# Optimization experiments

Measured on AMD Instinct MI355X. Metric: run time of the kernel, lower is better.

The kernel has to match this reference:

```python
import jax, jax.numpy as jnp
import numpy as np

HIDDEN = 1024

def _cat_linear(x, W, b, cat_ids):
    # x: (B,T,Din), W: (C,Din,Dout), b: (C,Dout)
    return jnp.einsum('bti,bio->bto', x, W[cat_ids]) + b[cat_ids][:, None, :]

def _sinusoidal(timesteps, dim):
    # timesteps: (B,T) int -> (B,T,dim)
    t = timesteps.astype(jnp.float32)
    half = dim // 2
    exponent = -jnp.arange(half, dtype=jnp.float32) * (jnp.log(10000.0) / half)
    freqs = t[..., None] * jnp.exp(exponent)
    return jnp.concatenate([jnp.sin(freqs), jnp.cos(freqs)], axis=-1)

def setup_inputs() -> dict:
    key = jax.random.key(0)
    ks = jax.random.split(key, 8)
    B, T, A, H, C = 64, 64, 64, HIDDEN, 16
    actions = jax.random.normal(ks[0], (B, T, A), dtype=jnp.float32)
    timesteps = jax.random.randint(ks[1], (B,), 0, 1000)
    cat_ids = jax.random.randint(ks[2], (B,), 0, C)
    W1 = 0.02 * jax.random.normal(ks[3], (C, A, H), dtype=jnp.float32)
    b1 = jnp.zeros((C, H), dtype=jnp.float32)
    W2 = 0.02 * jax.random.normal(ks[4], (C, 2 * H, H), dtype=jnp.float32)
    b2 = jnp.zeros((C, H), dtype=jnp.float32)
    W3 = 0.02 * jax.random.normal(ks[5], (C, H, H), dtype=jnp.float32)
    b3 = jnp.zeros((C, H), dtype=jnp.float32)
    return {"actions": actions, "timesteps": timesteps, "cat_ids": cat_ids,
            "W1": W1, "b1": b1, "W2": W2, "b2": b2, "W3": W3, "b3": b3}

def reference(actions, timesteps, cat_ids, W1, b1, W2, b2, W3, b3):
    B, T, _ = actions.shape
    ts = jnp.broadcast_to(timesteps[:, None], (B, T))  # (B,T)
    a_emb = _cat_linear(actions, W1, b1, cat_ids)        # (B,T,H)
    tau = _sinusoidal(ts, HIDDEN).astype(a_emb.dtype)    # (B,T,H)
    x = jnp.concatenate([a_emb, tau], axis=-1)           # (B,T,2H)
    h = _cat_linear(x, W2, b2, cat_ids)
    h = h * jax.nn.sigmoid(h)                            # swish
    return _cat_linear(h, W3, b3, cat_ids)               # (B,T,H)
```

## Files before the change

### kernel.cpp

```cpp
#include <hip/hip_runtime.h>
#include <math.h>


typedef short bf16x8 __attribute__((ext_vector_type(8)));
typedef float floatx4 __attribute__((ext_vector_type(4)));

__device__ inline short f2bf(float f) {
  union { float f; unsigned u; } v; v.f = f;
  unsigned u = v.u;
  return (short)(((u + 0x7fffu + ((u >> 16) & 1u)) >> 16) & 0xffffu);
}

__device__ __forceinline__ unsigned cvtpk(float a, float b) {
  unsigned r;
  asm("v_cvt_pk_bf16_f32 %0, %1, %2" : "=v"(r) : "v"(a), "v"(b));
  return r;
}

#if __has_builtin(__builtin_amdgcn_global_load_lds)
#define ASYNC_LDS 1
__device__ __forceinline__ void async16(const float* g, float* lds) {
  __builtin_amdgcn_global_load_lds(
      (const __attribute__((address_space(1))) unsigned int*)g,
      (__attribute__((address_space(3))) unsigned int*)lds, 16, 0, 0);
}
#else
#define ASYNC_LDS 0
__device__ __forceinline__ void async16(const float* g, float* lds) {
  *(floatx4*)lds = *(const floatx4*)g;
}
#endif

__device__ __forceinline__ void gload16(floatx4& d, const void* p) {
  asm volatile("global_load_dwordx4 %0, %1, off" : "=v"(d) : "v"(p) : "memory");
}
template<int N> __device__ __forceinline__ void vm_wait() {
  asm volatile("s_waitcnt vmcnt(%0)" :: "n"(N) : "memory");
}
__device__ __forceinline__ void lgkm0() {
  asm volatile("s_waitcnt lgkmcnt(0)" ::: "memory");
}

#define KBODY(VMX, LOADA, DOSTAGE, AIN, AOUT)                                  \
  {                                                                            \
    lgkm0();                                                                   \
    if (LOADA) {                                                               \
      _Pragma("unroll")                                                        \
      for (int mt = 0; mt < 8; ++mt) {                                         \
        const char* p = arow[mt] + aoff;                                       \
        if constexpr (A_F32) {                                                 \
          gload16(AOUT[2 * mt], p); gload16(AOUT[2 * mt + 1], p + 16);         \
        } else {                                                               \
          gload16(AOUT[mt], p);                                                \
        }                                                                      \
      }                                                                        \
      aoff += 32 * AB;                                                         \
    }                                                                          \
    if (DOSTAGE) {                                                             \
      _Pragma("unroll")                                                        \
      for (int i = 0; i < 4; ++i)                                              \
        async16((const float*)(wbp + goff[i]), bs + i * 256);                  \
      wbp += 32 * 1024 * 4;                                                    \
    }                                                                          \
    vm_wait<VMX>();                                                            \
    __builtin_amdgcn_sched_barrier(0);                                         \
    bf16x8 af[8];                                                              \
    _Pragma("unroll")                                                          \
    for (int mt = 0; mt < 8; ++mt) {                                           \
      if constexpr (A_F32) {                                                   \
        union { bf16x8 v; unsigned u[4]; } t;                                  \
        floatx4 x0 = AIN[2 * mt], x1 = AIN[2 * mt + 1];                        \
        t.u[0] = cvtpk(x0[0], x0[1]); t.u[1] = cvtpk(x0[2], x0[3]);            \
        t.u[2] = cvtpk(x1[0], x1[1]); t.u[3] = cvtpk(x1[2], x1[3]);            \
        af[mt] = t.v;                                                          \
      } else {                                                                 \
        union { floatx4 f; bf16x8 v; } t; t.f = AIN[mt]; af[mt] = t.v;         \
      }                                                                        \
    }                                                                          \
    _Pragma("unroll")                                                          \
    for (int nt = 0; nt < 2; ++nt) {                                           \
      const float* fp = bc + quad * 256 + ((nt * 16 + l16) ^ (quad << 3));     \
      float f[8];                                                              \
      _Pragma("unroll")                                                        \
      for (int j = 0; j < 8; ++j) f[j] = fp[j * 32];                           \
      union { bf16x8 v; unsigned u[4]; } bb;                                   \
      _Pragma("unroll")                                                        \
      for (int j = 0; j < 4; ++j) bb.u[j] = cvtpk(f[2 * j], f[2 * j + 1]);     \
      _Pragma("unroll")                                                        \
      for (int mt = 0; mt < 8; ++mt)                                           \
        acc[mt][nt] = __builtin_amdgcn_mfma_f32_16x16x32_bf16(                 \
            af[mt], bb.v, acc[mt][nt], 0, 0, 0);                               \
    }                                                                          \
    { float* t_ = bc; bc = bn; bn = bs; bs = t_; }                             \
  }

template<int K, bool A_F32, bool SWISH, bool OUT_BF16, bool TAU>
__global__ __launch_bounds__(256, 2) void gemm_kernel(
    const void* __restrict__ Aall, int lda,
    const float* __restrict__ Wall,
    const float* __restrict__ bias,
    const int* __restrict__ cat_ids,
    void* __restrict__ Out, int ldo,
    const int* __restrict__ ts)
{
  constexpr int NCOL = 1024;
  constexpr int KT = K / 32;
  constexpr int AB = A_F32 ? 4 : 2;
  constexpr int AOPS = A_F32 ? 16 : 8;
#if ASYNC_LDS
  constexpr int VM_MAIN = 8 + AOPS;
  constexpr int VM_T1   = 4 + AOPS;
#else
  constexpr int VM_MAIN = AOPS;
  constexpr int VM_T1   = AOPS;
#endif
  static_assert(KT >= 2 && ((KT - 2) % 2 == 0), "K must be a multiple of 64");
  (void)ts;

  __shared__ float slabs[4][3][1024];
  __shared__ int s_b[80], s_c[80], s_np;

  const int tid = threadIdx.x;
  if (tid < 80) { s_b[tid] = -1; s_c[tid] = 0; }
  __syncthreads();
  if (tid < 64) {
    const int myc = cat_ids[tid];
    int rank = 0, pst = 0, tot = 0;
    #pragma unroll
    for (int cc = 0; cc < 16; ++cc) {
      unsigned long long m = __ballot(myc == cc);
      const int cnt = __popcll(m);
      const int pc  = 2 * ((cnt + 1) >> 1);
      if (cc < myc)  pst += pc;
      if (cc == myc) rank = __popcll(m & ((1ull << tid) - 1ull));
      tot += pc;
    }
    const int slot = pst + rank;
    s_b[slot] = tid;
    s_c[slot] = myc;
    if (tid == 0) s_np = tot >> 1;
  }
  __syncthreads();

  const int e = blockIdx.y;
  if (e >= s_np) return;
  const int b0v = s_b[2 * e];
  int b1 = s_b[2 * e + 1];
  const int c = s_c[2 * e];
  const bool st1 = (b1 >= 0);
  if (!st1) b1 = b0v;

  const int wave = tid >> 6, lane = tid & 63;
  const int quad = lane >> 4, l16 = lane & 15;
  const int ns = blockIdx.x * 128;
  const int wcol = ns + wave * 32;

  const char* arow[8];
  #pragma unroll
  for (int mt = 0; mt < 8; ++mt) {
    const int pr = mt * 16 + l16;
    const int batch = (pr < 64) ? b0v : b1;
    const int row = batch * 64 + (pr & 63);
    arow[mt] = (const char*)Aall + (size_t)row * lda * AB;
  }

  int goff[4];
  #pragma unroll
  for (int i = 0; i < 4; ++i) {
    const int s  = i * 64 + lane;
    const int k  = s >> 3;
    const int c0 = ((s & 7) << 2) ^ ((s >> 6) << 3);
    goff[i] = (k * NCOL + c0) * 4;
  }

  float* const sl0 = &slabs[wave][0][0];
  float* const sl1 = &slabs[wave][1][0];
  float* const sl2 = &slabs[wave][2][0];
  float *bc = sl0, *bn = sl1, *bs = sl2;

  const char* wbp = (const char*)(Wall + (size_t)c * K * NCOL + wcol);

  floatx4 aA[A_F32 ? 16 : 8], aB[A_F32 ? 16 : 8];
  const int aq = quad * 8 * AB;

  #pragma unroll
  for (int mt = 0; mt < 8; ++mt) {
    const char* p = arow[mt] + aq;
    if constexpr (A_F32) { gload16(aA[2 * mt], p); gload16(aA[2 * mt + 1], p + 16); }
    else                 { gload16(aA[mt], p); }
  }
  #pragma unroll
  for (int i = 0; i < 4; ++i) async16((const float*)(wbp + goff[i]), sl0 + i * 256);
  wbp += 32 * NCOL * 4;
  #pragma unroll
  for (int i = 0; i < 4; ++i) async16((const float*)(wbp + goff[i]), sl1 + i * 256);
  wbp += 32 * NCOL * 4;

  int aoff = aq + 32 * AB;

  floatx4 acc[8][2];
  #pragma unroll
  for (int mt = 0; mt < 8; ++mt)
    #pragma unroll
    for (int nt = 0; nt < 2; ++nt)
      acc[mt][nt] = (floatx4){0.f, 0.f, 0.f, 0.f};

  for (int kt = 0; kt + 2 < KT; kt += 2) {
    KBODY(VM_MAIN, true, true, aA, aB);
    KBODY(VM_MAIN, true, true, aB, aA);
  }
  KBODY(VM_T1, true, false, aA, aB);
  KBODY(0, false, false, aB, aA);

  #pragma unroll
  for (int nt = 0; nt < 2; ++nt) {
    const int col = wcol + nt * 16 + l16;
    const float bv = bias[(size_t)c * NCOL + col];
    #pragma unroll
    for (int mt = 0; mt < 8; ++mt) {
      const int prb = mt * 16 + quad * 4;
      const int batch = (prb < 64) ? b0v : b1;
      const bool do_store = (prb < 64) || st1;
      #pragma unroll
      for (int r = 0; r < 4; ++r) {
        const int row = batch * 64 + ((prb + r) & 63);
        float v = acc[mt][nt][r] + bv;
        if constexpr (SWISH) v = v / (1.f + __expf(-v));
        if (do_store) {
          if constexpr (OUT_BF16)
            ((short*)Out)[(size_t)row * ldo + col] = f2bf(v);
          else
            ((float*)Out)[(size_t)row * ldo + col] = v;
        }
      }
    }
  }

  if constexpr (TAU) {
    const float t0  = (float)ts[b0v];
    const float t1v = (float)ts[b1];
    const int ic = ns + (tid & 127);
    const int hi = ic & 511;
    const float ef = __expf(-(float)hi * 0.017988946039015980f);
    float v0, v1;
    if (ic < 512) { v0 = sinf(t0 * ef); v1 = sinf(t1v * ef); }
    else          { v0 = cosf(t0 * ef); v1 = cosf(t1v * ef); }
    const short q0 = f2bf(v0), q1 = f2bf(v1);
    short* xp = (short*)Out;
    const int r0 = tid >> 7;
    #pragma unroll 4
    for (int rr = 0; rr < 32; ++rr) {
      const int rl = r0 + 2 * rr;
      xp[(size_t)(b0v * 64 + rl) * ldo + 1024 + ic] = q0;
      if (st1) xp[(size_t)(b1 * 64 + rl) * ldo + 1024 + ic] = q1;
    }
  }
}

extern "C" void kernel_launch(void* const* d_in, const int* in_sizes, int n_in,
                              void* d_out, int out_size, void* d_ws, size_t ws_size,
                              hipStream_t stream) {
  const float* actions   = (const float*)d_in[0];
  const int*   timesteps = (const int*)  d_in[1];
  const int*   cat_ids   = (const int*)  d_in[2];
  const float* W1 = (const float*)d_in[3];
  const float* B1 = (const float*)d_in[4];
  const float* W2 = (const float*)d_in[5];
  const float* B2 = (const float*)d_in[6];
  const float* W3 = (const float*)d_in[7];
  const float* B3 = (const float*)d_in[8];

  short* x = (short*)d_ws;
  short* h = x + (size_t)64 * 64 * 2048;

  dim3 grid(8, 40), blk(256);

  gemm_kernel<64, true, false, true, true><<<grid, blk, 0, stream>>>(
      (const void*)actions, 64, W1, B1, cat_ids, (void*)x, 2048, timesteps);
  gemm_kernel<2048, false, true, true, false><<<grid, blk, 0, stream>>>(
      (const void*)x, 2048, W2, B2, cat_ids, (void*)h, 1024, nullptr);
  gemm_kernel<1024, false, false, false, false><<<grid, blk, 0, stream>>>(
      (const void*)h, 1024, W3, B3, cat_ids, d_out, 1024, nullptr);
}
```

Before: 432.3 us.

## Load weights directly into registers and halve block size to two waves

Removes the LDS staging of weight tiles: each lane now loads its weight fragments straight from global memory with scalar-base plus vector-offset dword loads, double-buffered in registers. Blocks shrink to 128 threads covering 64 columns, and the grid doubles in x to keep the same coverage. The aim is to cut LDS traffic, its waits and its footprint so more blocks fit per CU. In exchange, the weight loads are strided dword loads rather than wide loads, and register pressure rises.

```diff
diff --git a/kernel.cpp b/kernel.cpp
--- a/kernel.cpp
+++ b/kernel.cpp
@@ -17,85 +17,77 @@
   return r;
 }
 
-#if __has_builtin(__builtin_amdgcn_global_load_lds)
-#define ASYNC_LDS 1
-__device__ __forceinline__ void async16(const float* g, float* lds) {
-  __builtin_amdgcn_global_load_lds(
-      (const __attribute__((address_space(1))) unsigned int*)g,
-      (__attribute__((address_space(3))) unsigned int*)lds, 16, 0, 0);
-}
-#else
-#define ASYNC_LDS 0
-__device__ __forceinline__ void async16(const float* g, float* lds) {
-  *(floatx4*)lds = *(const floatx4*)g;
-}
-#endif
-
-__device__ __forceinline__ void gload16(floatx4& d, const void* p) {
-  asm volatile("global_load_dwordx4 %0, %1, off" : "=v"(d) : "v"(p) : "memory");
-}
-template<int N> __device__ __forceinline__ void vm_wait() {
+template<int IMM>
+__device__ __forceinline__ void gdw(float& d, unsigned voff, unsigned long long base) {
+  asm volatile("global_load_dword %0, %1, %2 offset:%3"
+               : "=v"(d) : "v"(voff), "s"(base), "n"(IMM) : "memory");
+}
+template<int IMM>
+__device__ __forceinline__ void gdx4(floatx4& d, unsigned voff, unsigned long long base) {
+  asm volatile("global_load_dwordx4 %0, %1, %2 offset:%3"
+               : "=v"(d) : "v"(voff), "s"(base), "n"(IMM) : "memory");
+}
+template<int N>
+__device__ __forceinline__ void vm_wait() {
   asm volatile("s_waitcnt vmcnt(%0)" :: "n"(N) : "memory");
 }
-__device__ __forceinline__ void lgkm0() {
-  asm volatile("s_waitcnt lgkmcnt(0)" ::: "memory");
-}
-
-#define KBODY(VMX, LOADA, DOSTAGE, AIN, AOUT)                                  \
-  {                                                                            \
-    lgkm0();                                                                   \
-    if (LOADA) {                                                               \
-      _Pragma("unroll")                                                        \
-      for (int mt = 0; mt < 8; ++mt) {                                         \
-        const char* p = arow[mt] + aoff;                                       \
-        if constexpr (A_F32) {                                                 \
-          gload16(AOUT[2 * mt], p); gload16(AOUT[2 * mt + 1], p + 16);         \
-        } else {                                                               \
-          gload16(AOUT[mt], p);                                                \
-        }                                                                      \
-      }                                                                        \
-      aoff += 32 * AB;                                                         \
-    }                                                                          \
-    if (DOSTAGE) {                                                             \
-      _Pragma("unroll")                                                        \
-      for (int i = 0; i < 4; ++i)                                              \
-        async16((const float*)(wbp + goff[i]), bs + i * 256);                  \
-      wbp += 32 * 1024 * 4;                                                    \
-    }                                                                          \
-    vm_wait<VMX>();                                                            \
-    __builtin_amdgcn_sched_barrier(0);                                         \
-    bf16x8 af[8];                                                              \
-    _Pragma("unroll")                                                          \
-    for (int mt = 0; mt < 8; ++mt) {                                           \
-      if constexpr (A_F32) {                                                   \
-        union { bf16x8 v; unsigned u[4]; } t;                                  \
-        floatx4 x0 = AIN[2 * mt], x1 = AIN[2 * mt + 1];                        \
-        t.u[0] = cvtpk(x0[0], x0[1]); t.u[1] = cvtpk(x0[2], x0[3]);            \
-        t.u[2] = cvtpk(x1[0], x1[1]); t.u[3] = cvtpk(x1[2], x1[3]);            \
-        af[mt] = t.v;                                                          \
-      } else {                                                                 \
-        union { floatx4 f; bf16x8 v; } t; t.f = AIN[mt]; af[mt] = t.v;         \
-      }                                                                        \
-    }                                                                          \
-    _Pragma("unroll")                                                          \
-    for (int nt = 0; nt < 2; ++nt) {                                           \
-      const float* fp = bc + quad * 256 + ((nt * 16 + l16) ^ (quad << 3));     \
-      float f[8];                                                              \
-      _Pragma("unroll")                                                        \
-      for (int j = 0; j < 8; ++j) f[j] = fp[j * 32];                           \
-      union { bf16x8 v; unsigned u[4]; } bb;                                   \
-      _Pragma("unroll")                                                        \
-      for (int j = 0; j < 4; ++j) bb.u[j] = cvtpk(f[2 * j], f[2 * j + 1]);     \
-      _Pragma("unroll")                                                        \
-      for (int mt = 0; mt < 8; ++mt)                                           \
-        acc[mt][nt] = __builtin_amdgcn_mfma_f32_16x16x32_bf16(                 \
-            af[mt], bb.v, acc[mt][nt], 0, 0, 0);                               \
-    }                                                                          \
-    { float* t_ = bc; bc = bn; bn = bs; bs = t_; }                             \
-  }
+
+#define ISSUE_W(WBUF) do {                                                   \
+    _Pragma("unroll")                                                        \
+    for (int j = 0; j < 8; ++j) {                                            \
+      gdw<0 >(WBUF[j],     vW[j], Wq);                                       \
+      gdw<64>(WBUF[8 + j], vW[j], Wq);                                       \
+    }                                                                        \
+    Wq += 32ull * 1024 * 4;                                                  \
+  } while (0)
+
+#define ISSUE_A(ABUF) do {                                                   \
+    _Pragma("unroll")                                                        \
+    for (int mt = 0; mt < 8; ++mt) {                                         \
+      if constexpr (A_F32) {                                                 \
+        gdx4<0 >(ABUF[2 * mt],     vA[mt], Aq);                              \
+        gdx4<16>(ABUF[2 * mt + 1], vA[mt], Aq);                              \
+      } else {                                                               \
+        gdx4<0>(ABUF[mt], vA[mt], Aq);                                       \
+      }                                                                      \
+    }                                                                        \
+    Aq += 32ull * AB;                                                        \
+  } while (0)
+
+#define KSTEP(VM, AIN, AOUT, WIN, DO_A, DO_W) do {                           \
+    vm_wait<VM>();                                                           \
+    __builtin_amdgcn_sched_barrier(0);                                       \
+    union { bf16x8 v; unsigned u[4]; } wb0, wb1;                             \
+    _Pragma("unroll")                                                        \
+    for (int jj = 0; jj < 4; ++jj) {                                         \
+      wb0.u[jj] = cvtpk(WIN[2 * jj],     WIN[2 * jj + 1]);                   \
+      wb1.u[jj] = cvtpk(WIN[8 + 2 * jj], WIN[8 + 2 * jj + 1]);               \
+    }                                                                        \
+    bf16x8 af[8];                                                            \
+    _Pragma("unroll")                                                        \
+    for (int mt = 0; mt < 8; ++mt) {                                         \
+      if constexpr (A_F32) {                                                 \
+        union { bf16x8 v; unsigned u[4]; } t;                                \
+        floatx4 x0 = AIN[2 * mt], x1 = AIN[2 * mt + 1];                      \
+        t.u[0] = cvtpk(x0[0], x0[1]); t.u[1] = cvtpk(x0[2], x0[3]);          \
+        t.u[2] = cvtpk(x1[0], x1[1]); t.u[3] = cvtpk(x1[2], x1[3]);          \
+        af[mt] = t.v;                                                        \
+      } else {                                                               \
+        union { floatx4 f; bf16x8 v; } t; t.f = AIN[mt]; af[mt] = t.v;       \
+      }                                                                      \
+    }                                                                        \
+    __builtin_amdgcn_sched_barrier(0);                                       \
+    if (DO_A) ISSUE_A(AOUT);                                                 \
+    if (DO_W) ISSUE_W(WIN);                                                  \
+    _Pragma("unroll")                                                        \
+    for (int mt = 0; mt < 8; ++mt) {                                         \
+      acc[mt][0] = __builtin_amdgcn_mfma_f32_16x16x32_bf16(af[mt], wb0.v, acc[mt][0], 0, 0, 0); \
+      acc[mt][1] = __builtin_amdgcn_mfma_f32_16x16x32_bf16(af[mt], wb1.v, acc[mt][1], 0, 0, 0); \
+    }                                                                        \
+  } while (0)
 
 template<int K, bool A_F32, bool SWISH, bool OUT_BF16, bool TAU>
-__global__ __launch_bounds__(256, 2) void gemm_kernel(
+__global__ __launch_bounds__(128, 2) void gemm_kernel(
     const void* __restrict__ Aall, int lda,
     const float* __restrict__ Wall,
     const float* __restrict__ bias,
@@ -106,18 +98,9 @@
   constexpr int NCOL = 1024;
   constexpr int KT = K / 32;
   constexpr int AB = A_F32 ? 4 : 2;
-  constexpr int AOPS = A_F32 ? 16 : 8;
-#if ASYNC_LDS
-  constexpr int VM_MAIN = 8 + AOPS;
-  constexpr int VM_T1   = 4 + AOPS;
-#else
-  constexpr int VM_MAIN = AOPS;
-  constexpr int VM_T1   = AOPS;
-#endif
-  static_assert(KT >= 2 && ((KT - 2) % 2 == 0), "K must be a multiple of 64");
+  static_assert(KT >= 2 && ((KT - 2) % 2 == 0), "K must be multiple of 64");
   (void)ts;
 
-  __shared__ float slabs[4][3][1024];
   __shared__ int s_b[80], s_c[80], s_np;
 
   const int tid = threadIdx.x;
@@ -144,73 +127,68 @@
 
   const int e = blockIdx.y;
   if (e >= s_np) return;
-  const int b0v = s_b[2 * e];
-  int b1 = s_b[2 * e + 1];
-  const int c = s_c[2 * e];
+  const int b0v = __builtin_amdgcn_readfirstlane(s_b[2 * e]);
+  int b1        = __builtin_amdgcn_readfirstlane(s_b[2 * e + 1]);
+  const int c   = __builtin_amdgcn_readfirstlane(s_c[2 * e]);
   const bool st1 = (b1 >= 0);
   if (!st1) b1 = b0v;
 
   const int wave = tid >> 6, lane = tid & 63;
   const int quad = lane >> 4, l16 = lane & 15;
-  const int ns = blockIdx.x * 128;
+  const int ns = blockIdx.x * 64;
   const int wcol = ns + wave * 32;
 
-  const char* arow[8];
+  const unsigned wqoff = (unsigned)__builtin_amdgcn_readfirstlane(
+      (int)(((unsigned)c * (unsigned)K * NCOL + (unsigned)wcol) * 4u));
+  unsigned long long Wq = (unsigned long long)Wall + wqoff;
+  unsigned long long Aq = (unsigned long long)Aall;
+
+  unsigned vW[8];
+  #pragma unroll
+  for (int j = 0; j < 8; ++j)
+    vW[j] = (unsigned)((quad * 8 + j) * (NCOL * 4) + l16 * 4);
+
+  unsigned vA[8];
   #pragma unroll
   for (int mt = 0; mt < 8; ++mt) {
     const int pr = mt * 16 + l16;
     const int batch = (pr < 64) ? b0v : b1;
     const int row = batch * 64 + (pr & 63);
-    arow[mt] = (const char*)Aall + (size_t)row * lda * AB;
-  }
-
-  int goff[4];
-  #pragma unroll
-  for (int i = 0; i < 4; ++i) {
-    const int s  = i * 64 + lane;
-    const int k  = s >> 3;
-    const int c0 = ((s & 7) << 2) ^ ((s >> 6) << 3);
-    goff[i] = (k * NCOL + c0) * 4;
-  }
-
-  float* const sl0 = &slabs[wave][0][0];
-  float* const sl1 = &slabs[wave][1][0];
-  float* const sl2 = &slabs[wave][2][0];
-  float *bc = sl0, *bn = sl1, *bs = sl2;
-
-  const char* wbp = (const char*)(Wall + (size_t)c * K * NCOL + wcol);
-
-  floatx4 aA[A_F32 ? 16 : 8], aB[A_F32 ? 16 : 8];
-  const int aq = quad * 8 * AB;
-
+    vA[mt] = (unsigned)(row * lda * AB + quad * 8 * AB);
+  }
+
+  float wA[16], wB[16];
+  floatx4 aBuf0[A_F32 ? 16 : 8];
+  floatx4 aBuf1[A_F32 ? 1 : 8];
+
+  floatx4 acc[8][2];
   #pragma unroll
   for (int mt = 0; mt < 8; ++mt) {
-    const char* p = arow[mt] + aq;
-    if constexpr (A_F32) { gload16(aA[2 * mt], p); gload16(aA[2 * mt + 1], p + 16); }
-    else                 { gload16(aA[mt], p); }
-  }
-  #pragma unroll
-  for (int i = 0; i < 4; ++i) async16((const float*)(wbp + goff[i]), sl0 + i * 256);
-  wbp += 32 * NCOL * 4;
-  #pragma unroll
-  for (int i = 0; i < 4; ++i) async16((const float*)(wbp + goff[i]), sl1 + i * 256);
-  wbp += 32 * NCOL * 4;
-
-  int aoff = aq + 32 * AB;
-
-  floatx4 acc[8][2];
-  #pragma unroll
-  for (int mt = 0; mt < 8; ++mt)
-    #pragma unroll
-    for (int nt = 0; nt < 2; ++nt)
-      acc[mt][nt] = (floatx4){0.f, 0.f, 0.f, 0.f};
-
-  for (int kt = 0; kt + 2 < KT; kt += 2) {
-    KBODY(VM_MAIN, true, true, aA, aB);
-    KBODY(VM_MAIN, true, true, aB, aA);
-  }
-  KBODY(VM_T1, true, false, aA, aB);
-  KBODY(0, false, false, aB, aA);
+    acc[mt][0] = (floatx4){0.f, 0.f, 0.f, 0.f};
+    acc[mt][1] = (floatx4){0.f, 0.f, 0.f, 0.f};
+  }
+
+  ISSUE_W(wA);
+  ISSUE_A(aBuf0);
+  ISSUE_W(wB);
+
+  if constexpr (A_F32) {
+    #pragma unroll 1
+    for (int s = 0; s + 2 < KT; s += 2) {
+      KSTEP(16, aBuf0, aBuf0, wA, true, true);
+      KSTEP(16, aBuf0, aBuf0, wB, true, true);
+    }
+    KSTEP(16, aBuf0, aBuf0, wA, true, false);
+    KSTEP(0,  aBuf0, aBuf0, wB, false, false);
+  } else {
+    #pragma unroll 1
+    for (int s = 0; s + 2 < KT; s += 2) {
+      KSTEP(16, aBuf0, aBuf1, wA, true, true);
+      KSTEP(16, aBuf1, aBuf0, wB, true, true);
+    }
+    KSTEP(16, aBuf0, aBuf1, wA, true, false);
+    KSTEP(0,  aBuf1, aBuf1, wB, false, false);
+  }
 
   #pragma unroll
   for (int nt = 0; nt < 2; ++nt) {
@@ -239,7 +217,7 @@
   if constexpr (TAU) {
     const float t0  = (float)ts[b0v];
     const float t1v = (float)ts[b1];
-    const int ic = ns + (tid & 127);
+    const int ic = ns + (tid & 63);
     const int hi = ic & 511;
     const float ef = __expf(-(float)hi * 0.017988946039015980f);
     float v0, v1;
@@ -247,7 +225,7 @@
     else          { v0 = cosf(t0 * ef); v1 = cosf(t1v * ef); }
     const short q0 = f2bf(v0), q1 = f2bf(v1);
     short* xp = (short*)Out;
-    const int r0 = tid >> 7;
+    const int r0 = tid >> 6;
     #pragma unroll 4
     for (int rr = 0; rr < 32; ++rr) {
       const int rl = r0 + 2 * rr;
@@ -273,7 +251,7 @@
   short* x = (short*)d_ws;
   short* h = x + (size_t)64 * 64 * 2048;
 
-  dim3 grid(8, 40), blk(256);
+  dim3 grid(16, 40), blk(128);
 
   gemm_kernel<64, true, false, true, true><<<grid, blk, 0, stream>>>(
       (const void*)actions, 64, W1, B1, cat_ids, (void*)x, 2048, timesteps);
```

After: 406.8 us. 1.06x faster.
